# Performance work log

Hardware: AMD Instinct MI355X
Metric: run time of the kernel (lower is better)

The kernel has to match this reference:

```python
import jax, jax.numpy as jnp
import numpy as np

B, T, E, H = 2, 2048, 2048, 16
D = E // H


def setup_inputs() -> dict:
    key = jax.random.key(0)
    ks = jax.random.split(key, 5)
    s = 0.02
    return {
        "x": jax.random.normal(ks[0], (B, T, E), jnp.float32),
        "Wq": jax.random.normal(ks[1], (E, E), jnp.float32) * s,
        "Wk": jax.random.normal(ks[2], (E, E), jnp.float32) * s,
        "Wv": jax.random.normal(ks[3], (E, E), jnp.float32) * s,
        "Wp": jax.random.normal(ks[4], (E, E), jnp.float32) * s,
        "bp": jnp.zeros((E,), jnp.float32),
    }


def reference(x, Wq, Wk, Wv, Wp, bp):
    b, t, e = x.shape
    h, d = H, E // H
    # torch Linear: y = x @ W.T (no bias for qkv)
    Q = (x @ Wq.T).reshape(b, h, t, d)  # faithful: view without transpose
    K = (x @ Wk.T).reshape(b, h, t, d)
    V = (x @ Wv.T).reshape(b, h, t, d)
    scores = jnp.einsum("bhqd,bhkd->bhqk", Q, K)
    causal = jnp.triu(jnp.ones((t, t), bool), k=1)  # True above diagonal
    scores = jnp.where(causal, -jnp.inf, scores)
    weights = jax.nn.softmax(scores / jnp.sqrt(jnp.float32(d)), axis=-1)
    # dropout p=0.0 (eval) -> identity
    ctx = jnp.einsum("bhqk,bhkd->bhqd", weights, V)  # (b,h,t,d)
    ctx = ctx.transpose(0, 2, 1, 3).reshape(b, t, e)
    return ctx @ Wp.T + bp
```

## Files before the change

### kernel.cpp

```cpp
#include <hip/hip_runtime.h>

#define SEQ   2048
#define EMB   2048
#define NHEAD 16
#define HDIM  128
#define ROWSM 4096

typedef float  f32x4   __attribute__((ext_vector_type(4)));
typedef float  f32x16  __attribute__((ext_vector_type(16)));
typedef __bf16 bf16x8  __attribute__((ext_vector_type(8)));

__device__ __forceinline__ unsigned short f2bf(float f) {
  union { float f; unsigned int u; } v; v.f = f;
  return (unsigned short)((v.u + 0x7fffu + ((v.u >> 16) & 1u)) >> 16);
}
__device__ __forceinline__ unsigned int pk2(float a, float b) {
  return (unsigned int)f2bf(a) | ((unsigned int)f2bf(b) << 16);
}

__device__ __forceinline__ void gload16(const void* g, void* l) {
  __builtin_amdgcn_global_load_lds(
      (__attribute__((address_space(1))) const unsigned int*)g,
      (__attribute__((address_space(3))) unsigned int*)l,
      16, 0, 0);
}

__global__ void cvt_bf16(const float* __restrict__ in,
                         unsigned short* __restrict__ out, int n4) {
  int i = blockIdx.x * 256 + threadIdx.x;
  if (i >= n4) return;
  float4 v = ((const float4*)in)[i];
  ushort4 o;
  o.x = f2bf(v.x); o.y = f2bf(v.y); o.z = f2bf(v.z); o.w = f2bf(v.w);
  ((ushort4*)out)[i] = o;
}

template <int STORE_F32>
__global__ __launch_bounds__(256, 2) void gemm_nt(
    const unsigned short* __restrict__ A, const unsigned short* __restrict__ B,
    void* __restrict__ Cout, const float* __restrict__ bias,
    int M, int N, int K) {
  __shared__ __align__(16) unsigned short As[128 * 64];
  __shared__ __align__(16) unsigned short Bs[128 * 64];
  const int tid  = threadIdx.x;
  const int lane = tid & 63;
  const int w    = tid >> 6;
  const int m0 = blockIdx.y * 128;
  const int n0 = blockIdx.x * 128;
  const int wm = (w >> 1) * 64;
  const int wn = (w & 1) * 64;
  const int lg = lane >> 4;
  const int lc = lane & 15;

  f32x4 acc[4][4] = {};

  const int srow = lane >> 3;
  const int scol = (lane & 7) * 8;

  for (int k0 = 0; k0 < K; k0 += 64) {
    if (k0) __syncthreads();
#pragma unroll
    for (int ii = 0; ii < 4; ++ii) {
      int i = w * 4 + ii;
      int r = i * 8 + srow;
      gload16(A + (size_t)(m0 + r) * K + k0 + scol, (char*)As + i * 1024);
      gload16(B + (size_t)(n0 + r) * K + k0 + scol, (char*)Bs + i * 1024);
    }
    __syncthreads();
#pragma unroll
    for (int kk = 0; kk < 2; ++kk) {
      const int co = kk * 32 + lg * 8;
      bf16x8 a[4], b[4];
#pragma unroll
      for (int i = 0; i < 4; ++i)
        a[i] = *(const bf16x8*)(As + (wm + i * 16 + lc) * 64 + co);
#pragma unroll
      for (int j = 0; j < 4; ++j)
        b[j] = *(const bf16x8*)(Bs + (wn + j * 16 + lc) * 64 + co);
#pragma unroll
      for (int i = 0; i < 4; ++i)
#pragma unroll
        for (int j = 0; j < 4; ++j)
          acc[i][j] = __builtin_amdgcn_mfma_f32_16x16x32_bf16(a[i], b[j], acc[i][j], 0, 0, 0);
    }
  }

  const int rb = lg * 4;
#pragma unroll
  for (int i = 0; i < 4; ++i) {
#pragma unroll
    for (int j = 0; j < 4; ++j) {
      int col = n0 + wn + j * 16 + lc;
#pragma unroll
      for (int r = 0; r < 4; ++r) {
        int row = m0 + wm + i * 16 + rb + r;
        if (STORE_F32) {
          ((float*)Cout)[(size_t)row * N + col] = acc[i][j][r] + bias[col];
        } else {
          ((unsigned short*)Cout)[(size_t)row * N + col] = f2bf(acc[i][j][r]);
        }
      }
    }
  }
}

__global__ __launch_bounds__(256, 2) void attn_causal(
    const unsigned short* __restrict__ Pq, const unsigned short* __restrict__ Pk,
    const unsigned short* __restrict__ Pv, unsigned short* __restrict__ ctx) {
  __shared__ __align__(16) unsigned short Ks[64 * 128];
  __shared__ __align__(16) unsigned short Vt[128 * 64];

  const int tid  = threadIdx.x;
  const int lane = tid & 63;
  const int w    = tid >> 6;
  const int ql   = lane & 31;
  const int hi   = lane >> 5;
  const int lg   = lane >> 4;
  const int lc   = lane & 15;

  const int bh = blockIdx.y;
  const int b  = bh >> 4;
  const int h  = bh & 15;
  const int qt = (bh & 16) ? blockIdx.x : (15 - blockIdx.x);
  const int q0 = qt * 128;
  const int qw = q0 + w * 32;
  const int qg = qw + ql;

  const size_t hoff = (size_t)bh * SEQ * HDIM;
  const unsigned short* Q  = Pq + hoff;
  const unsigned short* Kh = Pk + hoff;
  const unsigned short* Vh = Pv + hoff;

  bf16x8 bq[8];
#pragma unroll
  for (int d8 = 0; d8 < 8; ++d8)
    bq[d8] = *(const bf16x8*)(Q + (size_t)qg * HDIM + d8 * 16 + hi * 8);

  const float NEG = -3.0e38f;
  f32x16 o[4];
#pragma unroll
  for (int dt = 0; dt < 4; ++dt)
#pragma unroll
    for (int r = 0; r < 16; ++r) o[dt][r] = 0.f;
  float m_r = NEG, l_r = 0.f;

  const float Cs   = 0.12753123161692858f;
  const float TDEF = 62.7f;

  const int ntiles = (q0 >> 6) + 2;
  for (int t = 0; t < ntiles; ++t) {
    const int kv0 = t * 64;
    if (t) __syncthreads();
#pragma unroll
    for (int ii = 0; ii < 4; ++ii) {
      int i = w * 4 + ii;
      int r = i * 4 + lg;
      int sd = lc ^ (r & 7);
      gload16(Kh + (size_t)(kv0 + r) * HDIM + sd * 8, (char*)Ks + i * 1024);
    }
#pragma unroll
    for (int uu = 0; uu < 2; ++uu) {
      int u = tid + uu * 256;
      int kp = u >> 4, dg = u & 15;
      int k = kp * 2, d0 = dg * 8;
      uint4 r0 = *(const uint4*)(Vh + (size_t)(kv0 + k) * HDIM + d0);
      uint4 r1 = *(const uint4*)(Vh + (size_t)(kv0 + k + 1) * HDIM + d0);
      const unsigned short* e0 = (const unsigned short*)&r0;
      const unsigned short* e1 = (const unsigned short*)&r1;
#pragma unroll
      for (int jj = 0; jj < 8; ++jj) {
        int d = d0 + jj;
        int slotswz = (k >> 3) ^ jj ^ (dg & 7);
        int byteoff = d * 128 + (slotswz << 4) + (k & 7) * 2;
        *(unsigned int*)((char*)Vt + byteoff) =
            (unsigned int)e0[jj] | ((unsigned int)e1[jj] << 16);
      }
    }
    __syncthreads();

    if (kv0 > qw + 31) continue;
    const bool s1on = (kv0 + 32 <= qw + 31);
    const bool diag = (kv0 + 63 > qw);

    f32x16 c0, c1;
#pragma unroll
    for (int r = 0; r < 16; ++r) { c0[r] = 0.f; c1[r] = s1on ? 0.f : NEG; }
#pragma unroll
    for (int d8 = 0; d8 < 8; ++d8) {
      bf16x8 ak = *(const bf16x8*)((const char*)Ks + ql * 256 +
                                   (((d8 * 2 + hi) ^ (ql & 7)) << 4));
      c0 = __builtin_amdgcn_mfma_f32_32x32x16_bf16(ak, bq[d8], c0, 0, 0, 0);
    }
    if (s1on) {
#pragma unroll
      for (int d8 = 0; d8 < 8; ++d8) {
        bf16x8 ak = *(const bf16x8*)((const char*)Ks + (32 + ql) * 256 +
                                     (((d8 * 2 + hi) ^ (ql & 7)) << 4));
        c1 = __builtin_amdgcn_mfma_f32_32x32x16_bf16(ak, bq[d8], c1, 0, 0, 0);
      }
    }
    if (diag) {
#pragma unroll
      for (int r = 0; r < 16; ++r) {
        int kvl = (r & 3) + 8 * (r >> 2) + 4 * hi;
        if (kv0 + kvl > qg) c0[r] = NEG;
        if (s1on && kv0 + 32 + kvl > qg) c1[r] = NEG;
      }
    }
    float rm = c0[0];
#pragma unroll
    for (int r = 1; r < 16; ++r) rm = fmaxf(rm, c0[r]);
#pragma unroll
    for (int r = 0; r < 16; ++r) rm = fmaxf(rm, c1[r]);
    rm = fmaxf(rm, __shfl_xor(rm, 32));

    if (__any(rm > m_r + TDEF)) {
      float mnew = fmaxf(m_r, rm);
      float alpha = exp2f((m_r - mnew) * Cs);
      m_r = mnew;
      l_r *= alpha;
#pragma unroll
      for (int r = 0; r < 16; ++r) {
        float ar = __shfl(alpha, (r & 3) + 8 * (r >> 2) + 4 * hi);
#pragma unroll
        for (int dt = 0; dt < 4; ++dt) o[dt][r] *= ar;
      }
    }
#pragma unroll
    for (int r = 0; r < 16; ++r) {
      c0[r] = exp2f((c0[r] - m_r) * Cs);
      c1[r] = exp2f((c1[r] - m_r) * Cs);
    }
    float ps = 0.f;
#pragma unroll
    for (int r = 0; r < 16; ++r) ps += c0[r] + c1[r];
    ps += __shfl_xor(ps, 32);
    l_r += ps;

    bf16x8 pa[4];
#pragma unroll
    for (int t4 = 0; t4 < 4; ++t4) {
      const f32x16& cc = (t4 < 2) ? c0 : c1;
      const int rA = (t4 & 1) * 8;
      unsigned int pkL0 = pk2(cc[rA + 0], cc[rA + 1]);
      unsigned int pkL1 = pk2(cc[rA + 2], cc[rA + 3]);
      unsigned int pkH0 = pk2(cc[rA + 4], cc[rA + 5]);
      unsigned int pkH1 = pk2(cc[rA + 6], cc[rA + 7]);
      unsigned int give0 = hi ? pkL0 : pkH0;
      unsigned int give1 = hi ? pkL1 : pkH1;
      unsigned int keep0 = hi ? pkH0 : pkL0;
      unsigned int keep1 = hi ? pkH1 : pkL1;
      unsigned int recv0 = __shfl_xor(give0, 32);
      unsigned int recv1 = __shfl_xor(give1, 32);
      union { unsigned int u[4]; bf16x8 v; } pu;
      pu.u[0] = hi ? recv0 : keep0;
      pu.u[1] = hi ? recv1 : keep1;
      pu.u[2] = hi ? keep0 : recv0;
      pu.u[3] = hi ? keep1 : recv1;
      pa[t4] = pu.v;
    }
#pragma unroll
    for (int t4 = 0; t4 < 4; ++t4) {
      if (diag && kv0 + t4 * 16 > qw + 31) continue;
#pragma unroll
      for (int dt = 0; dt < 4; ++dt) {
        int d = dt * 32 + ql;
        bf16x8 bv = *(const bf16x8*)((const char*)Vt + d * 128 +
                                     (((t4 * 2 + hi) ^ (d & 7) ^ ((d >> 3) & 7)) << 4));
        o[dt] = __builtin_amdgcn_mfma_f32_32x32x16_bf16(pa[t4], bv, o[dt], 0, 0, 0);
      }
    }
  }

  float linv = 1.0f / l_r;
  unsigned short* outp = ctx + (size_t)b * SEQ * EMB + (size_t)h * HDIM;
#pragma unroll
  for (int r = 0; r < 16; ++r) {
    int kvl = (r & 3) + 8 * (r >> 2) + 4 * hi;
    float lr = __shfl(linv, kvl);
    int qrow = qw + kvl;
#pragma unroll
    for (int dt = 0; dt < 4; ++dt)
      outp[(size_t)qrow * EMB + dt * 32 + ql] = f2bf(o[dt][r] * lr);
  }
}

extern "C" void kernel_launch(void* const* d_in, const int* in_sizes, int n_in,
                              void* d_out, int out_size, void* d_ws, size_t ws_size,
                              hipStream_t stream) {
  const float* x  = (const float*)d_in[0];
  const float* Wq = (const float*)d_in[1];
  const float* Wk = (const float*)d_in[2];
  const float* Wv = (const float*)d_in[3];
  const float* Wp = (const float*)d_in[4];
  const float* bp = (const float*)d_in[5];

  char* ws = (char*)d_ws;
  unsigned short* xb = (unsigned short*)ws;
  unsigned short* Wb = (unsigned short*)(ws + (size_t)(16u << 20));
  unsigned short* Pq = (unsigned short*)(ws + (size_t)(24u << 20));
  unsigned short* Pk = (unsigned short*)(ws + (size_t)(40u << 20));
  unsigned short* Pv = (unsigned short*)(ws + (size_t)(56u << 20));

  const int nX4 = ROWSM * EMB / 4;
  const int nW4 = EMB * EMB / 4;

  cvt_bf16<<<nX4 / 256, 256, 0, stream>>>(x, xb, nX4);

  dim3 ggrid(EMB / 128, ROWSM / 128);

  cvt_bf16<<<nW4 / 256, 256, 0, stream>>>(Wq, Wb, nW4);
  gemm_nt<0><<<ggrid, 256, 0, stream>>>(xb, Wb, Pq, nullptr, ROWSM, EMB, EMB);
  cvt_bf16<<<nW4 / 256, 256, 0, stream>>>(Wk, Wb, nW4);
  gemm_nt<0><<<ggrid, 256, 0, stream>>>(xb, Wb, Pk, nullptr, ROWSM, EMB, EMB);
  cvt_bf16<<<nW4 / 256, 256, 0, stream>>>(Wv, Wb, nW4);
  gemm_nt<0><<<ggrid, 256, 0, stream>>>(xb, Wb, Pv, nullptr, ROWSM, EMB, EMB);

  attn_causal<<<dim3(SEQ / 128, 32), 256, 0, stream>>>(Pq, Pk, Pv, xb);

  cvt_bf16<<<nW4 / 256, 256, 0, stream>>>(Wp, Wb, nW4);
  gemm_nt<1><<<ggrid, 256, 0, stream>>>(xb, Wb, d_out, bp, ROWSM, EMB, EMB);
}
```

Measured before the change: 305.4 us.

## Double-buffer attention K/V tiles, XCD-swizzle GEMM blocks, use native bf16 convert

The attention kernel now double-buffers K and V tiles in LDS and prefetches the next tile while computing the current one, so each tile needs one barrier instead of two. The MFMA sections are wrapped in s_setprio. The GEMMs switch to a 1D grid with a block-index swizzle that groups neighbouring tiles onto the same XCD to improve L2 reuse. f2bf now uses the native __bf16 conversion instead of manual rounding. The extra buffers double LDS use in attention (64KB per block), which may lower occupancy.

```diff
diff --git a/kernel.cpp b/kernel.cpp
--- a/kernel.cpp
+++ b/kernel.cpp
@@ -11,8 +11,7 @@
 typedef __bf16 bf16x8  __attribute__((ext_vector_type(8)));
 
 __device__ __forceinline__ unsigned short f2bf(float f) {
-  union { float f; unsigned int u; } v; v.f = f;
-  return (unsigned short)((v.u + 0x7fffu + ((v.u >> 16) & 1u)) >> 16);
+  union { __bf16 b; unsigned short u; } v; v.b = (__bf16)f; return v.u;
 }
 __device__ __forceinline__ unsigned int pk2(float a, float b) {
   return (unsigned int)f2bf(a) | ((unsigned int)f2bf(b) << 16);
@@ -45,8 +44,15 @@
   const int tid  = threadIdx.x;
   const int lane = tid & 63;
   const int w    = tid >> 6;
-  const int m0 = blockIdx.y * 128;
-  const int n0 = blockIdx.x * 128;
+
+  const int nwg = gridDim.x;
+  const int qq  = nwg >> 3;
+  const int wg  = blockIdx.x;
+  const int swz = (wg & 7) * qq + (wg >> 3);
+  const int tx  = N >> 7;
+  const int m0 = (swz / tx) * 128;
+  const int n0 = (swz % tx) * 128;
+
   const int wm = (w >> 1) * 64;
   const int wn = (w & 1) * 64;
   const int lg = lane >> 4;
@@ -107,8 +113,8 @@
 __global__ __launch_bounds__(256, 2) void attn_causal(
     const unsigned short* __restrict__ Pq, const unsigned short* __restrict__ Pk,
     const unsigned short* __restrict__ Pv, unsigned short* __restrict__ ctx) {
-  __shared__ __align__(16) unsigned short Ks[64 * 128];
-  __shared__ __align__(16) unsigned short Vt[128 * 64];
+  __shared__ __align__(16) unsigned short Ks[2][64 * 128];
+  __shared__ __align__(16) unsigned short Vt[2][128 * 64];
 
   const int tid  = threadIdx.x;
   const int lane = tid & 63;
@@ -147,129 +153,162 @@
   const float Cs   = 0.12753123161692858f;
   const float TDEF = 62.7f;
 
-  const int ntiles = (q0 >> 6) + 2;
-  for (int t = 0; t < ntiles; ++t) {
-    const int kv0 = t * 64;
-    if (t) __syncthreads();
+  auto stageK = [&](int buf, int kv0) {
 #pragma unroll
     for (int ii = 0; ii < 4; ++ii) {
       int i = w * 4 + ii;
       int r = i * 4 + lg;
       int sd = lc ^ (r & 7);
-      gload16(Kh + (size_t)(kv0 + r) * HDIM + sd * 8, (char*)Ks + i * 1024);
-    }
+      gload16(Kh + (size_t)(kv0 + r) * HDIM + sd * 8, (char*)&Ks[buf][0] + i * 1024);
+    }
+  };
+  auto loadV = [&](uint4* vr, int kv0) {
 #pragma unroll
     for (int uu = 0; uu < 2; ++uu) {
       int u = tid + uu * 256;
       int kp = u >> 4, dg = u & 15;
       int k = kp * 2, d0 = dg * 8;
-      uint4 r0 = *(const uint4*)(Vh + (size_t)(kv0 + k) * HDIM + d0);
-      uint4 r1 = *(const uint4*)(Vh + (size_t)(kv0 + k + 1) * HDIM + d0);
-      const unsigned short* e0 = (const unsigned short*)&r0;
-      const unsigned short* e1 = (const unsigned short*)&r1;
+      vr[uu * 2]     = *(const uint4*)(Vh + (size_t)(kv0 + k) * HDIM + d0);
+      vr[uu * 2 + 1] = *(const uint4*)(Vh + (size_t)(kv0 + k + 1) * HDIM + d0);
+    }
+  };
+  auto packV = [&](int buf, const uint4* vr) {
+#pragma unroll
+    for (int uu = 0; uu < 2; ++uu) {
+      int u = tid + uu * 256;
+      int kp = u >> 4, dg = u & 15;
+      int k = kp * 2, d0 = dg * 8;
+      const unsigned short* e0 = (const unsigned short*)&vr[uu * 2];
+      const unsigned short* e1 = (const unsigned short*)&vr[uu * 2 + 1];
 #pragma unroll
       for (int jj = 0; jj < 8; ++jj) {
         int d = d0 + jj;
         int slotswz = (k >> 3) ^ jj ^ (dg & 7);
         int byteoff = d * 128 + (slotswz << 4) + (k & 7) * 2;
-        *(unsigned int*)((char*)Vt + byteoff) =
+        *(unsigned int*)((char*)&Vt[buf][0] + byteoff) =
             (unsigned int)e0[jj] | ((unsigned int)e1[jj] << 16);
       }
     }
+  };
+
+  const int ntiles = (q0 >> 6) + 2;
+  uint4 vr[4];
+
+  stageK(0, 0);
+  loadV(vr, 0);
+  packV(0, vr);
+  __syncthreads();
+
+  int cur = 0;
+  for (int t = 0; t < ntiles; ++t) {
+    const int kv0 = t * 64;
+    const bool pf = (t + 1 < ntiles);
+    if (pf) { stageK(cur ^ 1, kv0 + 64); loadV(vr, kv0 + 64); }
+
+    if (kv0 <= qw + 31) {
+      const bool s1on = (kv0 + 32 <= qw + 31);
+      const bool diag = (kv0 + 63 > qw);
+      const char* ks = (const char*)&Ks[cur][0];
+      const char* vt = (const char*)&Vt[cur][0];
+
+      f32x16 c0, c1;
+#pragma unroll
+      for (int r = 0; r < 16; ++r) { c0[r] = 0.f; c1[r] = s1on ? 0.f : NEG; }
+      __builtin_amdgcn_s_setprio(1);
+#pragma unroll
+      for (int d8 = 0; d8 < 8; ++d8) {
+        bf16x8 ak = *(const bf16x8*)(ks + ql * 256 +
+                                     (((d8 * 2 + hi) ^ (ql & 7)) << 4));
+        c0 = __builtin_amdgcn_mfma_f32_32x32x16_bf16(ak, bq[d8], c0, 0, 0, 0);
+      }
+      if (s1on) {
+#pragma unroll
+        for (int d8 = 0; d8 < 8; ++d8) {
+          bf16x8 ak = *(const bf16x8*)(ks + (32 + ql) * 256 +
+                                       (((d8 * 2 + hi) ^ (ql & 7)) << 4));
+          c1 = __builtin_amdgcn_mfma_f32_32x32x16_bf16(ak, bq[d8], c1, 0, 0, 0);
+        }
+      }
+      __builtin_amdgcn_s_setprio(0);
+
+      if (diag) {
+#pragma unroll
+        for (int r = 0; r < 16; ++r) {
+          int kvl = (r & 3) + 8 * (r >> 2) + 4 * hi;
+          if (kv0 + kvl > qg) c0[r] = NEG;
+          if (s1on && kv0 + 32 + kvl > qg) c1[r] = NEG;
+        }
+      }
+      float rm = c0[0];
+#pragma unroll
+      for (int r = 1; r < 16; ++r) rm = fmaxf(rm, c0[r]);
+#pragma unroll
+      for (int r = 0; r < 16; ++r) rm = fmaxf(rm, c1[r]);
+      rm = fmaxf(rm, __shfl_xor(rm, 32));
+
+      if (__any(rm > m_r + TDEF)) {
+        float mnew = fmaxf(m_r, rm);
+        float alpha = exp2f((m_r - mnew) * Cs);
+        m_r = mnew;
+        l_r *= alpha;
+#pragma unroll
+        for (int r = 0; r < 16; ++r) {
+          float ar = __shfl(alpha, (r & 3) + 8 * (r >> 2) + 4 * hi);
+#pragma unroll
+          for (int dt = 0; dt < 4; ++dt) o[dt][r] *= ar;
+        }
+      }
+#pragma unroll
+      for (int r = 0; r < 16; ++r) {
+        c0[r] = exp2f((c0[r] - m_r) * Cs);
+        c1[r] = exp2f((c1[r] - m_r) * Cs);
+      }
+      float ps = 0.f;
+#pragma unroll
+      for (int r = 0; r < 16; ++r) ps += c0[r] + c1[r];
+      ps += __shfl_xor(ps, 32);
+      l_r += ps;
+
+      bf16x8 pa[4];
+#pragma unroll
+      for (int t4 = 0; t4 < 4; ++t4) {
+        const f32x16& cc = (t4 < 2) ? c0 : c1;
+        const int rA = (t4 & 1) * 8;
+        unsigned int pkL0 = pk2(cc[rA + 0], cc[rA + 1]);
+        unsigned int pkL1 = pk2(cc[rA + 2], cc[rA + 3]);
+        unsigned int pkH0 = pk2(cc[rA + 4], cc[rA + 5]);
+        unsigned int pkH1 = pk2(cc[rA + 6], cc[rA + 7]);
+        unsigned int give0 = hi ? pkL0 : pkH0;
+        unsigned int give1 = hi ? pkL1 : pkH1;
+        unsigned int keep0 = hi ? pkH0 : pkL0;
+        unsigned int keep1 = hi ? pkH1 : pkL1;
+        unsigned int recv0 = __shfl_xor(give0, 32);
+        unsigned int recv1 = __shfl_xor(give1, 32);
+        union { unsigned int u[4]; bf16x8 v; } pu;
+        pu.u[0] = hi ? recv0 : keep0;
+        pu.u[1] = hi ? recv1 : keep1;
+        pu.u[2] = hi ? keep0 : recv0;
+        pu.u[3] = hi ? keep1 : recv1;
+        pa[t4] = pu.v;
+      }
+      __builtin_amdgcn_s_setprio(1);
+#pragma unroll
+      for (int t4 = 0; t4 < 4; ++t4) {
+        if (diag && kv0 + t4 * 16 > qw + 31) continue;
+#pragma unroll
+        for (int dt = 0; dt < 4; ++dt) {
+          int d = dt * 32 + ql;
+          bf16x8 bv = *(const bf16x8*)(vt + d * 128 +
+                                       (((t4 * 2 + hi) ^ (d & 7) ^ ((d >> 3) & 7)) << 4));
+          o[dt] = __builtin_amdgcn_mfma_f32_32x32x16_bf16(pa[t4], bv, o[dt], 0, 0, 0);
+        }
+      }
+      __builtin_amdgcn_s_setprio(0);
+    }
+
+    if (pf) packV(cur ^ 1, vr);
     __syncthreads();
-
-    if (kv0 > qw + 31) continue;
-    const bool s1on = (kv0 + 32 <= qw + 31);
-    const bool diag = (kv0 + 63 > qw);
-
-    f32x16 c0, c1;
-#pragma unroll
-    for (int r = 0; r < 16; ++r) { c0[r] = 0.f; c1[r] = s1on ? 0.f : NEG; }
-#pragma unroll
-    for (int d8 = 0; d8 < 8; ++d8) {
-      bf16x8 ak = *(const bf16x8*)((const char*)Ks + ql * 256 +
-                                   (((d8 * 2 + hi) ^ (ql & 7)) << 4));
-      c0 = __builtin_amdgcn_mfma_f32_32x32x16_bf16(ak, bq[d8], c0, 0, 0, 0);
-    }
-    if (s1on) {
-#pragma unroll
-      for (int d8 = 0; d8 < 8; ++d8) {
-        bf16x8 ak = *(const bf16x8*)((const char*)Ks + (32 + ql) * 256 +
-                                     (((d8 * 2 + hi) ^ (ql & 7)) << 4));
-        c1 = __builtin_amdgcn_mfma_f32_32x32x16_bf16(ak, bq[d8], c1, 0, 0, 0);
-      }
-    }
-    if (diag) {
-#pragma unroll
-      for (int r = 0; r < 16; ++r) {
-        int kvl = (r & 3) + 8 * (r >> 2) + 4 * hi;
-        if (kv0 + kvl > qg) c0[r] = NEG;
-        if (s1on && kv0 + 32 + kvl > qg) c1[r] = NEG;
-      }
-    }
-    float rm = c0[0];
-#pragma unroll
-    for (int r = 1; r < 16; ++r) rm = fmaxf(rm, c0[r]);
-#pragma unroll
-    for (int r = 0; r < 16; ++r) rm = fmaxf(rm, c1[r]);
-    rm = fmaxf(rm, __shfl_xor(rm, 32));
-
-    if (__any(rm > m_r + TDEF)) {
-      float mnew = fmaxf(m_r, rm);
-      float alpha = exp2f((m_r - mnew) * Cs);
-      m_r = mnew;
-      l_r *= alpha;
-#pragma unroll
-      for (int r = 0; r < 16; ++r) {
-        float ar = __shfl(alpha, (r & 3) + 8 * (r >> 2) + 4 * hi);
-#pragma unroll
-        for (int dt = 0; dt < 4; ++dt) o[dt][r] *= ar;
-      }
-    }
-#pragma unroll
-    for (int r = 0; r < 16; ++r) {
-      c0[r] = exp2f((c0[r] - m_r) * Cs);
-      c1[r] = exp2f((c1[r] - m_r) * Cs);
-    }
-    float ps = 0.f;
-#pragma unroll
-    for (int r = 0; r < 16; ++r) ps += c0[r] + c1[r];
-    ps += __shfl_xor(ps, 32);
-    l_r += ps;
-
-    bf16x8 pa[4];
-#pragma unroll
-    for (int t4 = 0; t4 < 4; ++t4) {
-      const f32x16& cc = (t4 < 2) ? c0 : c1;
-      const int rA = (t4 & 1) * 8;
-      unsigned int pkL0 = pk2(cc[rA + 0], cc[rA + 1]);
-      unsigned int pkL1 = pk2(cc[rA + 2], cc[rA + 3]);
-      unsigned int pkH0 = pk2(cc[rA + 4], cc[rA + 5]);
-      unsigned int pkH1 = pk2(cc[rA + 6], cc[rA + 7]);
-      unsigned int give0 = hi ? pkL0 : pkH0;
-      unsigned int give1 = hi ? pkL1 : pkH1;
-      unsigned int keep0 = hi ? pkH0 : pkL0;
-      unsigned int keep1 = hi ? pkH1 : pkL1;
-      unsigned int recv0 = __shfl_xor(give0, 32);
-      unsigned int recv1 = __shfl_xor(give1, 32);
-      union { unsigned int u[4]; bf16x8 v; } pu;
-      pu.u[0] = hi ? recv0 : keep0;
-      pu.u[1] = hi ? recv1 : keep1;
-      pu.u[2] = hi ? keep0 : recv0;
-      pu.u[3] = hi ? keep1 : recv1;
-      pa[t4] = pu.v;
-    }
-#pragma unroll
-    for (int t4 = 0; t4 < 4; ++t4) {
-      if (diag && kv0 + t4 * 16 > qw + 31) continue;
-#pragma unroll
-      for (int dt = 0; dt < 4; ++dt) {
-        int d = dt * 32 + ql;
-        bf16x8 bv = *(const bf16x8*)((const char*)Vt + d * 128 +
-                                     (((t4 * 2 + hi) ^ (d & 7) ^ ((d >> 3) & 7)) << 4));
-        o[dt] = __builtin_amdgcn_mfma_f32_32x32x16_bf16(pa[t4], bv, o[dt], 0, 0, 0);
-      }
-    }
+    cur ^= 1;
   }
 
   float linv = 1.0f / l_r;
@@ -307,17 +346,17 @@
 
   cvt_bf16<<<nX4 / 256, 256, 0, stream>>>(x, xb, nX4);
 
-  dim3 ggrid(EMB / 128, ROWSM / 128);
+  const int ngemm = (EMB / 128) * (ROWSM / 128);
 
   cvt_bf16<<<nW4 / 256, 256, 0, stream>>>(Wq, Wb, nW4);
-  gemm_nt<0><<<ggrid, 256, 0, stream>>>(xb, Wb, Pq, nullptr, ROWSM, EMB, EMB);
+  gemm_nt<0><<<ngemm, 256, 0, stream>>>(xb, Wb, Pq, nullptr, ROWSM, EMB, EMB);
   cvt_bf16<<<nW4 / 256, 256, 0, stream>>>(Wk, Wb, nW4);
-  gemm_nt<0><<<ggrid, 256, 0, stream>>>(xb, Wb, Pk, nullptr, ROWSM, EMB, EMB);
+  gemm_nt<0><<<ngemm, 256, 0, stream>>>(xb, Wb, Pk, nullptr, ROWSM, EMB, EMB);
   cvt_bf16<<<nW4 / 256, 256, 0, stream>>>(Wv, Wb, nW4);
-  gemm_nt<0><<<ggrid, 256, 0, stream>>>(xb, Wb, Pv, nullptr, ROWSM, EMB, EMB);
+  gemm_nt<0><<<ngemm, 256, 0, stream>>>(xb, Wb, Pv, nullptr, ROWSM, EMB, EMB);
 
   attn_causal<<<dim3(SEQ / 128, 32), 256, 0, stream>>>(Pq, Pk, Pv, xb);
 
   cvt_bf16<<<nW4 / 256, 256, 0, stream>>>(Wp, Wb, nW4);
-  gemm_nt<1><<<ggrid, 256, 0, stream>>>(xb, Wb, d_out, bp, ROWSM, EMB, EMB);
-}
+  gemm_nt<1><<<ngemm, 256, 0, stream>>>(xb, Wb, d_out, bp, ROWSM, EMB, EMB);
+}
```

Result: slower. 338.4 us (+10.8%).
